# Optimization experiments

Hardware: AMD Instinct MI355X
Metric: run time of the kernel (lower is better)

Reference implementation:

```python
import jax, jax.numpy as jnp
import numpy as np

B, S, D, H = 2, 2048, 2048, 16
HD = D // H  # head_dim = 128


def setup_inputs() -> dict:
    key = jax.random.key(0)
    ks = jax.random.split(key, 9)
    s = 1.0 / np.sqrt(D)
    return {
        "x": jax.random.normal(ks[0], (B, S, D), jnp.float32),
        "Wq": jax.random.normal(ks[1], (D, D), jnp.float32) * s,
        "bq": jax.random.normal(ks[2], (D,), jnp.float32) * 0.02,
        "Wk": jax.random.normal(ks[3], (D, D), jnp.float32) * s,
        "bk": jax.random.normal(ks[4], (D,), jnp.float32) * 0.02,
        "Wv": jax.random.normal(ks[5], (D, D), jnp.float32) * s,
        "bv": jax.random.normal(ks[6], (D,), jnp.float32) * 0.02,
        "Wo": jax.random.normal(ks[7], (D, D), jnp.float32) * s,
        "bo": jax.random.normal(ks[8], (D,), jnp.float32) * 0.02,
    }


def reference(x, Wq, bq, Wk, bk, Wv, bv, Wo, bo):
    b, s, d = x.shape
    # nn.Linear: y = x @ W.T + b
    def split(t):
        # [b, s, d] -> [b, H, s, HD]
        return t.reshape(b, s, H, HD).transpose(0, 2, 1, 3)

    q = split(x @ Wq.T + bq)
    k = split(x @ Wk.T + bk)
    v = split(x @ Wv.T + bv)

    scale = jnp.asarray(HD, x.dtype) ** 0.5
    qk = jnp.einsum("bhqd,bhkd->bhqk", q, k) / scale  # [b, H, s, s]
    weights = jax.nn.softmax(qk, axis=-1)
    attn = jnp.einsum("bhqk,bhkd->bhqd", weights, v)  # [b, H, s, HD]

    merged = attn.transpose(0, 2, 1, 3).reshape(b, s, d)
    return merged @ Wo.T + bo
```

## Files before the change

kernel.cpp:

```cpp
#include <hip/hip_runtime.h>

typedef __bf16 bf16_t;
typedef bf16_t bf16x8 __attribute__((ext_vector_type(8)));
typedef bf16_t bf16x4 __attribute__((ext_vector_type(4)));
typedef float  f32x4  __attribute__((ext_vector_type(4)));

#define DDIM  2048
#define SEQ   2048
#define NH    16
#define HDIM  128
#define BATCH 2
#define MROWS (BATCH * SEQ)
#define XEL   ((size_t)MROWS * DDIM)

__device__ __forceinline__ void async_ld16(const bf16_t* g, bf16_t* l) {
  __builtin_amdgcn_global_load_lds(
      (const __attribute__((address_space(1))) void*)g,
      (__attribute__((address_space(3))) void*)l, 16, 0, 0);
}

__global__ void cvt_f32_bf16(const float* __restrict__ in,
                             bf16_t* __restrict__ out, int n) {
  int i = (blockIdx.x * blockDim.x + threadIdx.x) * 4;
  const int stride = gridDim.x * blockDim.x * 4;
  for (; i < n; i += stride) {
    const float4 v = *reinterpret_cast<const float4*>(in + i);
    bf16x4 o;
    o[0] = (bf16_t)v.x; o[1] = (bf16_t)v.y;
    o[2] = (bf16_t)v.z; o[3] = (bf16_t)v.w;
    *reinterpret_cast<bf16x4*>(out + i) = o;
  }
}

__global__ __launch_bounds__(512, 2) void gemm_qkv(
    const bf16_t* __restrict__ Ax, const bf16_t* __restrict__ Wcat,
    const float* __restrict__ bq, const float* __restrict__ bk,
    const float* __restrict__ bv,
    bf16_t* __restrict__ QKVh, float qscale) {
  __shared__ __align__(16) bf16_t sA[2][2][128 * 64];
  __shared__ __align__(16) bf16_t sB[2][192 * 64];

  const int tid  = threadIdx.x;
  const int lane = tid & 63;
  const int w    = tid >> 6;
  const int wm   = w >> 2;
  const int wn   = w & 3;
  const int lg   = lane >> 4;
  const int lr   = lane & 15;

  const int bid = blockIdx.x;
  const int l   = (bid & 7) * 64 + (bid >> 3);
  const int tm  = l & 15;
  const int tn  = l >> 4;
  const int row0  = tm * 256;
  const int ncol0 = tn * 192;

  auto stA = [&](int buf, int ha, int kt) {
#pragma unroll
    for (int L = 0; L < 2; ++L) {
      const int c = L * 512 + tid, r = c >> 3, ch = c & 7;
      async_ld16(Ax + (size_t)(row0 + ha * 128 + r) * DDIM + kt * 64 +
                     ((ch ^ (r & 7)) * 8),
                 &sA[buf][ha][c * 8]);
    }
  };
  auto stB = [&](int buf, int kt) {
#pragma unroll
    for (int L = 0; L < 3; ++L) {
      const int c = L * 512 + tid, r = c >> 3, ch = c & 7;
      async_ld16(Wcat + (size_t)(ncol0 + r) * DDIM + kt * 64 +
                     ((ch ^ (r & 7)) * 8),
                 &sB[buf][c * 8]);
    }
  };
  auto ldA = [&](int buf, int mf, int k) {
    const int row = mf * 16 + lr;
    const int ch  = (k * 4 + lg) ^ (row & 7);
    return *reinterpret_cast<const bf16x8*>(&sA[buf][wm][row * 64 + ch * 8]);
  };
  auto ldB = [&](int buf, int nf, int k) {
    const int row = wn * 48 + nf * 16 + lr;
    const int ch  = (k * 4 + lg) ^ (row & 7);
    return *reinterpret_cast<const bf16x8*>(&sB[buf][row * 64 + ch * 8]);
  };

  f32x4  acc[8][3] = {};
  bf16x8 bfr[3][2];

#define GPH(BUF, Q, LOADB, STAGE_STMT, VMW)                                   \
  {                                                                           \
    bf16x8 a00 = ldA(BUF, 2 * (Q), 0), a01 = ldA(BUF, 2 * (Q), 1);            \
    bf16x8 a10 = ldA(BUF, 2 * (Q) + 1, 0), a11 = ldA(BUF, 2 * (Q) + 1, 1);    \
    if (LOADB) {                                                              \
      _Pragma("unroll") for (int nf = 0; nf < 3; ++nf) {                      \
        bfr[nf][0] = ldB(BUF, nf, 0);                                         \
        bfr[nf][1] = ldB(BUF, nf, 1);                                         \
      }                                                                       \
    }                                                                         \
    STAGE_STMT;                                                               \
    if (VMW) asm volatile("s_waitcnt vmcnt(3)" ::: "memory");                 \
    __builtin_amdgcn_s_barrier();                                             \
    asm volatile("s_waitcnt lgkmcnt(0)" ::: "memory");                        \
    __builtin_amdgcn_sched_barrier(0);                                        \
    __builtin_amdgcn_s_setprio(1);                                            \
    _Pragma("unroll") for (int k = 0; k < 2; ++k) {                           \
      const bf16x8 A0 = k ? a01 : a00;                                        \
      const bf16x8 A1 = k ? a11 : a10;                                        \
      _Pragma("unroll") for (int nf = 0; nf < 3; ++nf) {                      \
        acc[2 * (Q)][nf] = __builtin_amdgcn_mfma_f32_16x16x32_bf16(           \
            A0, bfr[nf][k], acc[2 * (Q)][nf], 0, 0, 0);                       \
        acc[2 * (Q) + 1][nf] = __builtin_amdgcn_mfma_f32_16x16x32_bf16(       \
            A1, bfr[nf][k], acc[2 * (Q) + 1][nf], 0, 0, 0);                   \
      }                                                                       \
    }                                                                         \
    __builtin_amdgcn_s_setprio(0);                                            \
    __builtin_amdgcn_s_barrier();                                             \
  }

  stA(0, 0, 0); stA(0, 1, 0);
  stB(0, 0);
  stB(1, 1);
  asm volatile("s_waitcnt vmcnt(3)" ::: "memory");
  __builtin_amdgcn_s_barrier();

  for (int i = 0; i < 16; ++i) {
    const int t1 = (2 * i + 1) & 31;
    const int t2 = (2 * i + 2) & 31;
    const int t3 = (2 * i + 3) & 31;
    GPH(0, 0, true,  { stA(1, 0, t1); stA(1, 1, t1); }, 0)
    GPH(0, 1, false, { stB(0, t2); },                   0)
    GPH(0, 2, false, {},                                0)
    GPH(0, 3, false, {},                                1)
    GPH(1, 0, true,  { stA(0, 0, t2); stA(0, 1, t2); }, 0)
    GPH(1, 1, false, { stB(1, t3); },                   0)
    GPH(1, 2, false, {},                                0)
    GPH(1, 3, false, {},                                1)
  }
#undef GPH
  asm volatile("s_waitcnt vmcnt(0)" ::: "memory");

#pragma unroll
  for (int mf = 0; mf < 8; ++mf) {
    const int rr0 = row0 + wm * 128 + mf * 16 + lg * 4;
#pragma unroll
    for (int nf = 0; nf < 3; ++nf) {
      const int col = ncol0 + wn * 48 + nf * 16 + lr;
      const int mat = col >> 11;
      const int c2  = col & (DDIM - 1);
      const float bs = ((mat == 0) ? bq : (mat == 1) ? bk : bv)[c2];
      const float sc = (mat == 0) ? qscale : 1.0f;
      const int h = c2 >> 7, hd = c2 & (HDIM - 1);
      bf16_t* outb = QKVh + (size_t)mat * XEL;
#pragma unroll
      for (int r = 0; r < 4; ++r) {
        const int rr = rr0 + r;
        const int b = rr >> 11, s = rr & (SEQ - 1);
        outb[(((size_t)(b * NH + h)) * SEQ + s) * HDIM + hd] =
            (bf16_t)((acc[mf][nf][r] + bs) * sc);
      }
    }
  }
}

template <int OUTMODE>
__global__ __launch_bounds__(256) void gemm_bt(
    const bf16_t* __restrict__ A, const bf16_t* __restrict__ Bw,
    const float* __restrict__ bias, void* __restrict__ outp,
    int M, int N, int K, float scale) {
  __shared__ __align__(16) bf16_t sA[2][128 * 32];
  __shared__ __align__(16) bf16_t sB[2][128 * 32];

  const int tid  = threadIdx.x;
  const int lane = tid & 63;
  const int w    = tid >> 6;
  const int wm   = w >> 1;
  const int wn   = w & 1;
  const int lg   = lane >> 4;
  const int lr   = lane & 15;
  const int row0 = blockIdx.y * 128;
  const int col0 = blockIdx.x * 128;

  const int srow = tid >> 2;
  const int scol = (tid & 3) * 8;

  const bf16_t* gA = A  + (size_t)(row0 + srow) * K + scol;
  const bf16_t* gB = Bw + (size_t)(col0 + srow) * K + scol;

  f32x4 acc[4][4] = {};

  auto stage = [&](int buf, int k0) {
    async_ld16(gA + k0,                  &sA[buf][tid * 8]);
    async_ld16(gA + 64 * (size_t)K + k0, &sA[buf][(256 + tid) * 8]);
    async_ld16(gB + k0,                  &sB[buf][tid * 8]);
    async_ld16(gB + 64 * (size_t)K + k0, &sB[buf][(256 + tid) * 8]);
  };

  stage(0, 0);
  __syncthreads();

  int cur = 0;
  const int NT = K / 32;
  for (int t = 0; t < NT; ++t) {
    if (t + 1 < NT) stage(cur ^ 1, (t + 1) * 32);
    bf16x8 af[4], bfr[4];
#pragma unroll
    for (int i = 0; i < 4; ++i) {
      af[i]  = *reinterpret_cast<const bf16x8*>(
          &sA[cur][(wm * 64 + i * 16 + lr) * 32 + lg * 8]);
      bfr[i] = *reinterpret_cast<const bf16x8*>(
          &sB[cur][(wn * 64 + i * 16 + lr) * 32 + lg * 8]);
    }
#pragma unroll
    for (int i = 0; i < 4; ++i)
#pragma unroll
      for (int j = 0; j < 4; ++j)
        acc[i][j] = __builtin_amdgcn_mfma_f32_16x16x32_bf16(
            af[i], bfr[j], acc[i][j], 0, 0, 0);
    __syncthreads();
    cur ^= 1;
  }

#pragma unroll
  for (int i = 0; i < 4; ++i) {
    const int rowb = row0 + wm * 64 + i * 16 + lg * 4;
#pragma unroll
    for (int j = 0; j < 4; ++j) {
      const int col = col0 + wn * 64 + j * 16 + lr;
      const float bs = bias[col];
#pragma unroll
      for (int r = 0; r < 4; ++r) {
        const float v = (acc[i][j][r] + bs) * scale;
        const int rr = rowb + r;
        if (OUTMODE == 2) {
          ((float*)outp)[(size_t)rr * N + col] = v;
        } else {
          const int b  = rr >> 11;
          const int s  = rr & (SEQ - 1);
          const int h  = col >> 7;
          const int hd = col & (HDIM - 1);
          ((bf16_t*)outp)[(((size_t)(b * NH + h)) * SEQ + s) * HDIM + hd] =
              (bf16_t)v;
        }
      }
    }
  }
}

__global__ __launch_bounds__(256) void transpose_v(
    const bf16_t* __restrict__ Vp, bf16_t* __restrict__ Vt) {
  __shared__ __align__(16) bf16_t tt[64][72];
  const int bh = blockIdx.z;
  const int s0 = blockIdx.x * 64;
  const int d0 = blockIdx.y * 64;
  const int t  = threadIdx.x;
#pragma unroll
  for (int c = 0; c < 2; ++c) {
    const int r   = (c * 256 + t) >> 3;
    const int col = (t & 7) * 8;
    bf16x8 v = *reinterpret_cast<const bf16x8*>(
        Vp + ((size_t)bh * SEQ + s0 + r) * HDIM + d0 + col);
    *reinterpret_cast<bf16x8*>(&tt[r][col]) = v;
  }
  __syncthreads();
#pragma unroll
  for (int c = 0; c < 2; ++c) {
    const int dr = (c * 256 + t) >> 3;
    const int sc = (t & 7) * 8;
    bf16x8 o;
#pragma unroll
    for (int i = 0; i < 8; ++i) o[i] = tt[sc + i][dr];
    *reinterpret_cast<bf16x8*>(
        Vt + ((size_t)bh * HDIM + d0 + dr) * SEQ + s0 + sc) = o;
  }
}

__global__ __launch_bounds__(256) void attn_fwd(
    const bf16_t* __restrict__ Q, const bf16_t* __restrict__ K,
    const bf16_t* __restrict__ Vt, bf16_t* __restrict__ out) {
  __shared__ __align__(16) bf16_t sK[64 * 128];
  __shared__ __align__(16) bf16_t sV[128 * 64];
  __shared__ __align__(16) bf16_t sP[4][32][72];

  const int tid  = threadIdx.x;
  const int lane = tid & 63;
  const int w    = tid >> 6;
  const int lg   = lane >> 4;
  const int lr   = lane & 15;

  const int bid     = blockIdx.x;
  const int logical = (bid & 7) * 64 + (bid >> 3);
  const int bh      = logical >> 4;
  const int q0      = (logical & 15) * 128;
  const int qw      = q0 + w * 32;

  const bf16_t* Kb = K  + (size_t)bh * SEQ * HDIM;
  const bf16_t* Vb = Vt + (size_t)bh * HDIM * SEQ;

  bf16x8 qf[2][4];
#pragma unroll
  for (int mf = 0; mf < 2; ++mf) {
    const bf16_t* qbase = Q + ((size_t)bh * SEQ + qw + mf * 16 + lr) * HDIM;
#pragma unroll
    for (int kc = 0; kc < 4; ++kc)
      qf[mf][kc] = *reinterpret_cast<const bf16x8*>(qbase + kc * 32 + lg * 8);
  }

  bf16x8 onesf;
#pragma unroll
  for (int i = 0; i < 8; ++i) onesf[i] = (bf16_t)1.0f;

  f32x4 o[2][8] = {};
  f32x4 o1[2] = {};

  for (int kv0 = 0; kv0 < SEQ; kv0 += 64) {
    __syncthreads();
#pragma unroll
    for (int p = 0; p < 4; ++p) {
      const int slot = p * 256 + tid;
      const int kr = slot >> 4, kc = slot & 15;
      async_ld16(Kb + ((size_t)(kv0 + kr)) * HDIM + ((kc ^ (kr & 7)) * 8),
                 sK + slot * 8);
      const int vr = slot >> 3, vc = slot & 7;
      async_ld16(Vb + (size_t)vr * SEQ + kv0 + ((vc ^ (vr & 7)) * 8),
                 sV + slot * 8);
    }
    __syncthreads();

    f32x4 s[2][4] = {};
    __builtin_amdgcn_s_setprio(1);
#pragma unroll
    for (int kc = 0; kc < 4; ++kc) {
#pragma unroll
      for (int cb = 0; cb < 4; ++cb) {
        const int r  = cb * 16 + lr;
        const int ch = kc * 4 + lg;
        bf16x8 kf = *reinterpret_cast<const bf16x8*>(
            sK + r * 128 + ((ch ^ (r & 7)) * 8));
        s[0][cb] = __builtin_amdgcn_mfma_f32_16x16x32_bf16(qf[0][kc], kf, s[0][cb], 0, 0, 0);
        s[1][cb] = __builtin_amdgcn_mfma_f32_16x16x32_bf16(qf[1][kc], kf, s[1][cb], 0, 0, 0);
      }
    }
    __builtin_amdgcn_s_setprio(0);

#pragma unroll
    for (int mf = 0; mf < 2; ++mf)
#pragma unroll
      for (int r = 0; r < 4; ++r)
#pragma unroll
        for (int cb = 0; cb < 4; ++cb) {
          const float p = __builtin_amdgcn_exp2f(s[mf][cb][r]);
          sP[w][mf * 16 + lg * 4 + r][cb * 16 + lr] = (bf16_t)p;
        }

    asm volatile("s_waitcnt lgkmcnt(0)" ::: "memory");

    __builtin_amdgcn_s_setprio(1);
#pragma unroll
    for (int ks = 0; ks < 2; ++ks) {
      bf16x8 pf0 = *reinterpret_cast<const bf16x8*>(&sP[w][lr][ks * 32 + lg * 8]);
      bf16x8 pf1 = *reinterpret_cast<const bf16x8*>(&sP[w][16 + lr][ks * 32 + lg * 8]);
      o1[0] = __builtin_amdgcn_mfma_f32_16x16x32_bf16(pf0, onesf, o1[0], 0, 0, 0);
      o1[1] = __builtin_amdgcn_mfma_f32_16x16x32_bf16(pf1, onesf, o1[1], 0, 0, 0);
#pragma unroll
      for (int ob = 0; ob < 8; ++ob) {
        const int r  = ob * 16 + lr;
        const int ch = ks * 4 + lg;
        bf16x8 vf = *reinterpret_cast<const bf16x8*>(
            sV + r * 64 + ((ch ^ (r & 7)) * 8));
        o[0][ob] = __builtin_amdgcn_mfma_f32_16x16x32_bf16(pf0, vf, o[0][ob], 0, 0, 0);
        o[1][ob] = __builtin_amdgcn_mfma_f32_16x16x32_bf16(pf1, vf, o[1][ob], 0, 0, 0);
      }
    }
    __builtin_amdgcn_s_setprio(0);
  }

  const int b = bh >> 4, h = bh & 15;
#pragma unroll
  for (int mf = 0; mf < 2; ++mf) {
#pragma unroll
    for (int r = 0; r < 4; ++r) {
      const float inv_l = 1.0f / o1[mf][r];
      const int row = qw + mf * 16 + lg * 4 + r;
      bf16_t* obase = out + ((size_t)b * SEQ + row) * DDIM + h * HDIM;
#pragma unroll
      for (int ob = 0; ob < 8; ++ob)
        obase[ob * 16 + lr] = (bf16_t)(o[mf][ob][r] * inv_l);
    }
  }
}

extern "C" void kernel_launch(void* const* d_in, const int* in_sizes, int n_in,
                              void* d_out, int out_size, void* d_ws,
                              size_t ws_size, hipStream_t stream) {
  const float* x  = (const float*)d_in[0];
  const float* Wq = (const float*)d_in[1];
  const float* bq = (const float*)d_in[2];
  const float* Wk = (const float*)d_in[3];
  const float* bk = (const float*)d_in[4];
  const float* Wv = (const float*)d_in[5];
  const float* bv = (const float*)d_in[6];
  const float* Wo = (const float*)d_in[7];
  const float* bo = (const float*)d_in[8];

  bf16_t* ws = (bf16_t*)d_ws;
  const size_t XE = XEL;
  const size_t WE = (size_t)DDIM * DDIM;
  bf16_t* xb  = ws;
  bf16_t* wqb = ws + XE;
  bf16_t* wkb = wqb + WE;
  bf16_t* wvb = wkb + WE;
  bf16_t* wob = wvb + WE;
  bf16_t* Qh  = wob + WE;
  bf16_t* Kh  = Qh + XE;
  bf16_t* Vh  = Kh + XE;
  bf16_t* Vt  = Vh + XE;
  bf16_t* merged = xb;

  cvt_f32_bf16<<<4096, 256, 0, stream>>>(x, xb, (int)XE);
  cvt_f32_bf16<<<2048, 256, 0, stream>>>(Wq, wqb, (int)WE);
  cvt_f32_bf16<<<2048, 256, 0, stream>>>(Wk, wkb, (int)WE);
  cvt_f32_bf16<<<2048, 256, 0, stream>>>(Wv, wvb, (int)WE);
  cvt_f32_bf16<<<2048, 256, 0, stream>>>(Wo, wob, (int)WE);

  const float qscale = 0.12751744520778695f;

  gemm_qkv<<<512, 512, 0, stream>>>(xb, wqb, bq, bk, bv, Qh, qscale);

  transpose_v<<<dim3(SEQ / 64, HDIM / 64, BATCH * NH), 256, 0, stream>>>(Vh, Vt);

  attn_fwd<<<512, 256, 0, stream>>>(Qh, Kh, Vt, merged);

  dim3 gg(DDIM / 128, MROWS / 128);
  gemm_bt<2><<<gg, 256, 0, stream>>>(merged, wob, bo, d_out, MROWS, DDIM, DDIM, 1.0f);
}
```

Baseline: 276.1 us.

## Fuse conversions, triple-buffer QKV GEMM B tiles, rewrite output projection GEMM

Merges the five fp32-to-bf16 conversion launches into a single grid-stride kernel over all inputs. The QKV GEMM now triple-buffers its weight tile with a per-k-step loop that interleaves LDS fragment loads with MFMA groups through partial lgkmcnt waits. Its warp layout changes from 2x4 to 4x2, giving each wave a 64x96 sub-tile. The output projection GEMM is replaced by a 256x128-tile, 512-thread kernel with swizzled LDS, global_load_lds staging and the same pipeline, in place of the simple double-buffered 128x128 one. This costs more LDS per block, which may reduce occupancy.

```diff
diff --git a/kernel.cpp b/kernel.cpp
--- a/kernel.cpp
+++ b/kernel.cpp
@@ -12,6 +12,7 @@
 #define BATCH 2
 #define MROWS (BATCH * SEQ)
 #define XEL   ((size_t)MROWS * DDIM)
+#define WEL   ((size_t)DDIM * DDIM)
 
 __device__ __forceinline__ void async_ld16(const bf16_t* g, bf16_t* l) {
   __builtin_amdgcn_global_load_lds(
@@ -19,18 +20,50 @@
       (__attribute__((address_space(3))) void*)l, 16, 0, 0);
 }
 
-__global__ void cvt_f32_bf16(const float* __restrict__ in,
-                             bf16_t* __restrict__ out, int n) {
-  int i = (blockIdx.x * blockDim.x + threadIdx.x) * 4;
-  const int stride = gridDim.x * blockDim.x * 4;
-  for (; i < n; i += stride) {
-    const float4 v = *reinterpret_cast<const float4*>(in + i);
+__global__ void cvt_all(const float* __restrict__ x,
+                        const float* __restrict__ w0,
+                        const float* __restrict__ w1,
+                        const float* __restrict__ w2,
+                        const float* __restrict__ w3,
+                        bf16_t* __restrict__ ox, bf16_t* __restrict__ ow) {
+  const size_t CX = XEL / 4;
+  const size_t CW = WEL / 4;
+  const size_t total = CX + 4 * CW;
+  size_t c = (size_t)blockIdx.x * blockDim.x + threadIdx.x;
+  const size_t stride = (size_t)gridDim.x * blockDim.x;
+  for (; c < total; c += stride) {
+    float4 v;
+    bf16_t* outp;
+    if (c < CX) {
+      v = reinterpret_cast<const float4*>(x)[c];
+      outp = ox + c * 4;
+    } else {
+      const size_t d = c - CX;
+      const size_t seg = d >> 20;
+      const float* w = seg == 0 ? w0 : seg == 1 ? w1 : seg == 2 ? w2 : w3;
+      v = reinterpret_cast<const float4*>(w)[d & (CW - 1)];
+      outp = ow + d * 4;
+    }
     bf16x4 o;
     o[0] = (bf16_t)v.x; o[1] = (bf16_t)v.y;
     o[2] = (bf16_t)v.z; o[3] = (bf16_t)v.w;
-    *reinterpret_cast<bf16x4*>(out + i) = o;
-  }
-}
+    *reinterpret_cast<bf16x4*>(outp) = o;
+  }
+}
+
+#define QMM(NF, BV)                                                           \
+  __builtin_amdgcn_s_setprio(1);                                              \
+  _Pragma("unroll") for (int mf = 0; mf < 4; ++mf) {                          \
+    acc[mf][NF] = __builtin_amdgcn_mfma_f32_16x16x32_bf16(                    \
+        a_[mf][0], BV[0], acc[mf][NF], 0, 0, 0);                              \
+    acc[mf][NF] = __builtin_amdgcn_mfma_f32_16x16x32_bf16(                    \
+        a_[mf][1], BV[1], acc[mf][NF], 0, 0, 0);                              \
+  }                                                                           \
+  __builtin_amdgcn_s_setprio(0);
+
+#define LGKM(N)                                                               \
+  asm volatile("s_waitcnt lgkmcnt(" #N ")" ::: "memory");                     \
+  __builtin_amdgcn_sched_barrier(0);
 
 __global__ __launch_bounds__(512, 2) void gemm_qkv(
     const bf16_t* __restrict__ Ax, const bf16_t* __restrict__ Wcat,
@@ -38,137 +71,7 @@
     const float* __restrict__ bv,
     bf16_t* __restrict__ QKVh, float qscale) {
   __shared__ __align__(16) bf16_t sA[2][2][128 * 64];
-  __shared__ __align__(16) bf16_t sB[2][192 * 64];
-
-  const int tid  = threadIdx.x;
-  const int lane = tid & 63;
-  const int w    = tid >> 6;
-  const int wm   = w >> 2;
-  const int wn   = w & 3;
-  const int lg   = lane >> 4;
-  const int lr   = lane & 15;
-
-  const int bid = blockIdx.x;
-  const int l   = (bid & 7) * 64 + (bid >> 3);
-  const int tm  = l & 15;
-  const int tn  = l >> 4;
-  const int row0  = tm * 256;
-  const int ncol0 = tn * 192;
-
-  auto stA = [&](int buf, int ha, int kt) {
-#pragma unroll
-    for (int L = 0; L < 2; ++L) {
-      const int c = L * 512 + tid, r = c >> 3, ch = c & 7;
-      async_ld16(Ax + (size_t)(row0 + ha * 128 + r) * DDIM + kt * 64 +
-                     ((ch ^ (r & 7)) * 8),
-                 &sA[buf][ha][c * 8]);
-    }
-  };
-  auto stB = [&](int buf, int kt) {
-#pragma unroll
-    for (int L = 0; L < 3; ++L) {
-      const int c = L * 512 + tid, r = c >> 3, ch = c & 7;
-      async_ld16(Wcat + (size_t)(ncol0 + r) * DDIM + kt * 64 +
-                     ((ch ^ (r & 7)) * 8),
-                 &sB[buf][c * 8]);
-    }
-  };
-  auto ldA = [&](int buf, int mf, int k) {
-    const int row = mf * 16 + lr;
-    const int ch  = (k * 4 + lg) ^ (row & 7);
-    return *reinterpret_cast<const bf16x8*>(&sA[buf][wm][row * 64 + ch * 8]);
-  };
-  auto ldB = [&](int buf, int nf, int k) {
-    const int row = wn * 48 + nf * 16 + lr;
-    const int ch  = (k * 4 + lg) ^ (row & 7);
-    return *reinterpret_cast<const bf16x8*>(&sB[buf][row * 64 + ch * 8]);
-  };
-
-  f32x4  acc[8][3] = {};
-  bf16x8 bfr[3][2];
-
-#define GPH(BUF, Q, LOADB, STAGE_STMT, VMW)                                   \
-  {                                                                           \
-    bf16x8 a00 = ldA(BUF, 2 * (Q), 0), a01 = ldA(BUF, 2 * (Q), 1);            \
-    bf16x8 a10 = ldA(BUF, 2 * (Q) + 1, 0), a11 = ldA(BUF, 2 * (Q) + 1, 1);    \
-    if (LOADB) {                                                              \
-      _Pragma("unroll") for (int nf = 0; nf < 3; ++nf) {                      \
-        bfr[nf][0] = ldB(BUF, nf, 0);                                         \
-        bfr[nf][1] = ldB(BUF, nf, 1);                                         \
-      }                                                                       \
-    }                                                                         \
-    STAGE_STMT;                                                               \
-    if (VMW) asm volatile("s_waitcnt vmcnt(3)" ::: "memory");                 \
-    __builtin_amdgcn_s_barrier();                                             \
-    asm volatile("s_waitcnt lgkmcnt(0)" ::: "memory");                        \
-    __builtin_amdgcn_sched_barrier(0);                                        \
-    __builtin_amdgcn_s_setprio(1);                                            \
-    _Pragma("unroll") for (int k = 0; k < 2; ++k) {                           \
-      const bf16x8 A0 = k ? a01 : a00;                                        \
-      const bf16x8 A1 = k ? a11 : a10;                                        \
-      _Pragma("unroll") for (int nf = 0; nf < 3; ++nf) {                      \
-        acc[2 * (Q)][nf] = __builtin_amdgcn_mfma_f32_16x16x32_bf16(           \
-            A0, bfr[nf][k], acc[2 * (Q)][nf], 0, 0, 0);                       \
-        acc[2 * (Q) + 1][nf] = __builtin_amdgcn_mfma_f32_16x16x32_bf16(       \
-            A1, bfr[nf][k], acc[2 * (Q) + 1][nf], 0, 0, 0);                   \
-      }                                                                       \
-    }                                                                         \
-    __builtin_amdgcn_s_setprio(0);                                            \
-    __builtin_amdgcn_s_barrier();                                             \
-  }
-
-  stA(0, 0, 0); stA(0, 1, 0);
-  stB(0, 0);
-  stB(1, 1);
-  asm volatile("s_waitcnt vmcnt(3)" ::: "memory");
-  __builtin_amdgcn_s_barrier();
-
-  for (int i = 0; i < 16; ++i) {
-    const int t1 = (2 * i + 1) & 31;
-    const int t2 = (2 * i + 2) & 31;
-    const int t3 = (2 * i + 3) & 31;
-    GPH(0, 0, true,  { stA(1, 0, t1); stA(1, 1, t1); }, 0)
-    GPH(0, 1, false, { stB(0, t2); },                   0)
-    GPH(0, 2, false, {},                                0)
-    GPH(0, 3, false, {},                                1)
-    GPH(1, 0, true,  { stA(0, 0, t2); stA(0, 1, t2); }, 0)
-    GPH(1, 1, false, { stB(1, t3); },                   0)
-    GPH(1, 2, false, {},                                0)
-    GPH(1, 3, false, {},                                1)
-  }
-#undef GPH
-  asm volatile("s_waitcnt vmcnt(0)" ::: "memory");
-
-#pragma unroll
-  for (int mf = 0; mf < 8; ++mf) {
-    const int rr0 = row0 + wm * 128 + mf * 16 + lg * 4;
-#pragma unroll
-    for (int nf = 0; nf < 3; ++nf) {
-      const int col = ncol0 + wn * 48 + nf * 16 + lr;
-      const int mat = col >> 11;
-      const int c2  = col & (DDIM - 1);
-      const float bs = ((mat == 0) ? bq : (mat == 1) ? bk : bv)[c2];
-      const float sc = (mat == 0) ? qscale : 1.0f;
-      const int h = c2 >> 7, hd = c2 & (HDIM - 1);
-      bf16_t* outb = QKVh + (size_t)mat * XEL;
-#pragma unroll
-      for (int r = 0; r < 4; ++r) {
-        const int rr = rr0 + r;
-        const int b = rr >> 11, s = rr & (SEQ - 1);
-        outb[(((size_t)(b * NH + h)) * SEQ + s) * HDIM + hd] =
-            (bf16_t)((acc[mf][nf][r] + bs) * sc);
-      }
-    }
-  }
-}
-
-template <int OUTMODE>
-__global__ __launch_bounds__(256) void gemm_bt(
-    const bf16_t* __restrict__ A, const bf16_t* __restrict__ Bw,
-    const float* __restrict__ bias, void* __restrict__ outp,
-    int M, int N, int K, float scale) {
-  __shared__ __align__(16) bf16_t sA[2][128 * 32];
-  __shared__ __align__(16) bf16_t sB[2][128 * 32];
+  __shared__ __align__(16) bf16_t sB[3][192 * 64];
 
   const int tid  = threadIdx.x;
   const int lane = tid & 63;
@@ -177,71 +80,228 @@
   const int wn   = w & 1;
   const int lg   = lane >> 4;
   const int lr   = lane & 15;
-  const int row0 = blockIdx.y * 128;
-  const int col0 = blockIdx.x * 128;
-
-  const int srow = tid >> 2;
-  const int scol = (tid & 3) * 8;
-
-  const bf16_t* gA = A  + (size_t)(row0 + srow) * K + scol;
-  const bf16_t* gB = Bw + (size_t)(col0 + srow) * K + scol;
+
+  const int bid = blockIdx.x;
+  const int l   = (bid & 7) * 64 + (bid >> 3);
+  const int tm  = l & 15;
+  const int tn  = l >> 4;
+  const int row0  = tm * 256;
+  const int ncol0 = tn * 192;
+
+  auto stA = [&](int buf, int ha, int kt) {
+#pragma unroll
+    for (int L = 0; L < 2; ++L) {
+      const int c = L * 512 + tid, r = c >> 3, ch = c & 7;
+      async_ld16(Ax + (size_t)(row0 + ha * 128 + r) * DDIM + kt * 64 +
+                     ((ch ^ (r & 7)) * 8),
+                 &sA[buf][ha][c * 8]);
+    }
+  };
+  auto stB = [&](int buf, int kt) {
+#pragma unroll
+    for (int L = 0; L < 3; ++L) {
+      const int c = L * 512 + tid, r = c >> 3, ch = c & 7;
+      async_ld16(Wcat + (size_t)(ncol0 + r) * DDIM + kt * 64 +
+                     ((ch ^ (r & 7)) * 8),
+                 &sB[buf][c * 8]);
+    }
+  };
+  auto ldA = [&](int buf, int mf, int k) {
+    const int row = (wm & 1) * 64 + mf * 16 + lr;
+    const int ch  = (k * 4 + lg) ^ (row & 7);
+    return *reinterpret_cast<const bf16x8*>(
+        &sA[buf][wm >> 1][row * 64 + ch * 8]);
+  };
+  auto ldB = [&](int buf, int nf, int k) {
+    const int row = wn * 96 + nf * 16 + lr;
+    const int ch  = (k * 4 + lg) ^ (row & 7);
+    return *reinterpret_cast<const bf16x8*>(&sB[buf][row * 64 + ch * 8]);
+  };
+
+  f32x4 acc[4][6] = {};
+
+  stA(0, 0, 0); stA(0, 1, 0);
+  stB(0, 0);
+  stB(1, 1);
+  asm volatile("s_waitcnt vmcnt(3)" ::: "memory");
+  __builtin_amdgcn_s_barrier();
+
+  int bc = 0;
+  for (int t = 0; t < 32; ++t) {
+    const int p   = t & 1;
+    const int pn  = p ^ 1;
+    const int tn1 = (t + 1) & 31, tn2 = (t + 2) & 31;
+    const int b2i = bc == 0 ? 2 : bc - 1;
+
+    bf16x8 a_[4][2];
+#pragma unroll
+    for (int mf = 0; mf < 4; ++mf) {
+      a_[mf][0] = ldA(p, mf, 0);
+      a_[mf][1] = ldA(p, mf, 1);
+    }
+    bf16x8 b0[2], b1[2], b2[2], b3[2], b4[2], b5[2];
+    b0[0] = ldB(bc, 0, 0); b0[1] = ldB(bc, 0, 1);
+    b1[0] = ldB(bc, 1, 0); b1[1] = ldB(bc, 1, 1);
+    __builtin_amdgcn_sched_barrier(0);
+    stA(pn, 0, tn1); stA(pn, 1, tn1);
+    stB(b2i, tn2);
+    __builtin_amdgcn_sched_barrier(0);
+    LGKM(2)
+    QMM(0, b0)
+    b2[0] = ldB(bc, 2, 0); b2[1] = ldB(bc, 2, 1);
+    __builtin_amdgcn_sched_barrier(0);
+    LGKM(2)
+    QMM(1, b1)
+    b3[0] = ldB(bc, 3, 0); b3[1] = ldB(bc, 3, 1);
+    __builtin_amdgcn_sched_barrier(0);
+    LGKM(2)
+    QMM(2, b2)
+    b4[0] = ldB(bc, 4, 0); b4[1] = ldB(bc, 4, 1);
+    __builtin_amdgcn_sched_barrier(0);
+    LGKM(2)
+    QMM(3, b3)
+    b5[0] = ldB(bc, 5, 0); b5[1] = ldB(bc, 5, 1);
+    __builtin_amdgcn_sched_barrier(0);
+    LGKM(2)
+    QMM(4, b4)
+    LGKM(0)
+    QMM(5, b5)
+    asm volatile("s_waitcnt vmcnt(3)" ::: "memory");
+    __builtin_amdgcn_s_barrier();
+    bc = bc == 2 ? 0 : bc + 1;
+  }
+  asm volatile("s_waitcnt vmcnt(0)" ::: "memory");
+
+#pragma unroll
+  for (int mf = 0; mf < 4; ++mf) {
+    const int rr0 = row0 + wm * 64 + mf * 16 + lg * 4;
+#pragma unroll
+    for (int nf = 0; nf < 6; ++nf) {
+      const int col = ncol0 + wn * 96 + nf * 16 + lr;
+      const int mat = col >> 11;
+      const int c2  = col & (DDIM - 1);
+      const float bs = ((mat == 0) ? bq : (mat == 1) ? bk : bv)[c2];
+      const float sc = (mat == 0) ? qscale : 1.0f;
+      const int h = c2 >> 7, hd = c2 & (HDIM - 1);
+      bf16_t* outb = QKVh + (size_t)mat * XEL;
+#pragma unroll
+      for (int r = 0; r < 4; ++r) {
+        const int rr = rr0 + r;
+        const int b = rr >> 11, s = rr & (SEQ - 1);
+        outb[(((size_t)(b * NH + h)) * SEQ + s) * HDIM + hd] =
+            (bf16_t)((acc[mf][nf][r] + bs) * sc);
+      }
+    }
+  }
+}
+
+__global__ __launch_bounds__(512, 2) void gemm_bt(
+    const bf16_t* __restrict__ A, const bf16_t* __restrict__ Bw,
+    const float* __restrict__ bias, float* __restrict__ outp) {
+  __shared__ __align__(16) bf16_t sA[2][2][128 * 64];
+  __shared__ __align__(16) bf16_t sB[3][128 * 64];
+
+  const int tid  = threadIdx.x;
+  const int lane = tid & 63;
+  const int w    = tid >> 6;
+  const int wm   = w >> 1;
+  const int wn   = w & 1;
+  const int lg   = lane >> 4;
+  const int lr   = lane & 15;
+
+  const int bid = blockIdx.x;
+  const int l   = (bid & 7) * 32 + (bid >> 3);
+  const int tm  = l & 15;
+  const int tn  = l >> 4;
+  const int row0 = tm * 256;
+  const int col0 = tn * 128;
+
+  auto stA = [&](int buf, int ha, int kt) {
+#pragma unroll
+    for (int L = 0; L < 2; ++L) {
+      const int c = L * 512 + tid, r = c >> 3, ch = c & 7;
+      async_ld16(A + (size_t)(row0 + ha * 128 + r) * DDIM + kt * 64 +
+                     ((ch ^ (r & 7)) * 8),
+                 &sA[buf][ha][c * 8]);
+    }
+  };
+  auto stB = [&](int buf, int kt) {
+#pragma unroll
+    for (int L = 0; L < 2; ++L) {
+      const int c = L * 512 + tid, r = c >> 3, ch = c & 7;
+      async_ld16(Bw + (size_t)(col0 + r) * DDIM + kt * 64 +
+                     ((ch ^ (r & 7)) * 8),
+                 &sB[buf][c * 8]);
+    }
+  };
+  auto ldA = [&](int buf, int mf, int k) {
+    const int row = (wm & 1) * 64 + mf * 16 + lr;
+    const int ch  = (k * 4 + lg) ^ (row & 7);
+    return *reinterpret_cast<const bf16x8*>(
+        &sA[buf][wm >> 1][row * 64 + ch * 8]);
+  };
+  auto ldB = [&](int buf, int nf, int k) {
+    const int row = wn * 64 + nf * 16 + lr;
+    const int ch  = (k * 4 + lg) ^ (row & 7);
+    return *reinterpret_cast<const bf16x8*>(&sB[buf][row * 64 + ch * 8]);
+  };
 
   f32x4 acc[4][4] = {};
 
-  auto stage = [&](int buf, int k0) {
-    async_ld16(gA + k0,                  &sA[buf][tid * 8]);
-    async_ld16(gA + 64 * (size_t)K + k0, &sA[buf][(256 + tid) * 8]);
-    async_ld16(gB + k0,                  &sB[buf][tid * 8]);
-    async_ld16(gB + 64 * (size_t)K + k0, &sB[buf][(256 + tid) * 8]);
-  };
-
-  stage(0, 0);
-  __syncthreads();
-
-  int cur = 0;
-  const int NT = K / 32;
-  for (int t = 0; t < NT; ++t) {
-    if (t + 1 < NT) stage(cur ^ 1, (t + 1) * 32);
-    bf16x8 af[4], bfr[4];
-#pragma unroll
-    for (int i = 0; i < 4; ++i) {
-      af[i]  = *reinterpret_cast<const bf16x8*>(
-          &sA[cur][(wm * 64 + i * 16 + lr) * 32 + lg * 8]);
-      bfr[i] = *reinterpret_cast<const bf16x8*>(
-          &sB[cur][(wn * 64 + i * 16 + lr) * 32 + lg * 8]);
-    }
-#pragma unroll
-    for (int i = 0; i < 4; ++i)
-#pragma unroll
-      for (int j = 0; j < 4; ++j)
-        acc[i][j] = __builtin_amdgcn_mfma_f32_16x16x32_bf16(
-            af[i], bfr[j], acc[i][j], 0, 0, 0);
-    __syncthreads();
-    cur ^= 1;
-  }
-
-#pragma unroll
-  for (int i = 0; i < 4; ++i) {
-    const int rowb = row0 + wm * 64 + i * 16 + lg * 4;
-#pragma unroll
-    for (int j = 0; j < 4; ++j) {
-      const int col = col0 + wn * 64 + j * 16 + lr;
+  stA(0, 0, 0); stA(0, 1, 0);
+  stB(0, 0);
+  stB(1, 1);
+  asm volatile("s_waitcnt vmcnt(2)" ::: "memory");
+  __builtin_amdgcn_s_barrier();
+
+  int bc = 0;
+  for (int t = 0; t < 32; ++t) {
+    const int p   = t & 1;
+    const int pn  = p ^ 1;
+    const int tn1 = (t + 1) & 31, tn2 = (t + 2) & 31;
+    const int b2i = bc == 0 ? 2 : bc - 1;
+
+    bf16x8 a_[4][2];
+#pragma unroll
+    for (int mf = 0; mf < 4; ++mf) {
+      a_[mf][0] = ldA(p, mf, 0);
+      a_[mf][1] = ldA(p, mf, 1);
+    }
+    bf16x8 b0[2], b1[2], b2[2], b3[2];
+    b0[0] = ldB(bc, 0, 0); b0[1] = ldB(bc, 0, 1);
+    b1[0] = ldB(bc, 1, 0); b1[1] = ldB(bc, 1, 1);
+    __builtin_amdgcn_sched_barrier(0);
+    stA(pn, 0, tn1); stA(pn, 1, tn1);
+    stB(b2i, tn2);
+    __builtin_amdgcn_sched_barrier(0);
+    LGKM(2)
+    QMM(0, b0)
+    b2[0] = ldB(bc, 2, 0); b2[1] = ldB(bc, 2, 1);
+    __builtin_amdgcn_sched_barrier(0);
+    LGKM(2)
+    QMM(1, b1)
+    b3[0] = ldB(bc, 3, 0); b3[1] = ldB(bc, 3, 1);
+    __builtin_amdgcn_sched_barrier(0);
+    LGKM(2)
+    QMM(2, b2)
+    LGKM(0)
+    QMM(3, b3)
+    asm volatile("s_waitcnt vmcnt(2)" ::: "memory");
+    __builtin_amdgcn_s_barrier();
+    bc = bc == 2 ? 0 : bc + 1;
+  }
+  asm volatile("s_waitcnt vmcnt(0)" ::: "memory");
+
+#pragma unroll
+  for (int mf = 0; mf < 4; ++mf) {
+    const int row = row0 + wm * 64 + mf * 16 + lg * 4;
+#pragma unroll
+    for (int nf = 0; nf < 4; ++nf) {
+      const int col = col0 + wn * 64 + nf * 16 + lr;
       const float bs = bias[col];
 #pragma unroll
-      for (int r = 0; r < 4; ++r) {
-        const float v = (acc[i][j][r] + bs) * scale;
-        const int rr = rowb + r;
-        if (OUTMODE == 2) {
-          ((float*)outp)[(size_t)rr * N + col] = v;
-        } else {
-          const int b  = rr >> 11;
-          const int s  = rr & (SEQ - 1);
-          const int h  = col >> 7;
-          const int hd = col & (HDIM - 1);
-          ((bf16_t*)outp)[(((size_t)(b * NH + h)) * SEQ + s) * HDIM + hd] =
-              (bf16_t)v;
-        }
-      }
+      for (int r = 0; r < 4; ++r)
+        outp[(size_t)(row + r) * DDIM + col] = acc[mf][nf][r] + bs;
     }
   }
 }
@@ -404,7 +464,7 @@
 
   bf16_t* ws = (bf16_t*)d_ws;
   const size_t XE = XEL;
-  const size_t WE = (size_t)DDIM * DDIM;
+  const size_t WE = WEL;
   bf16_t* xb  = ws;
   bf16_t* wqb = ws + XE;
   bf16_t* wkb = wqb + WE;
@@ -416,11 +476,7 @@
   bf16_t* Vt  = Vh + XE;
   bf16_t* merged = xb;
 
-  cvt_f32_bf16<<<4096, 256, 0, stream>>>(x, xb, (int)XE);
-  cvt_f32_bf16<<<2048, 256, 0, stream>>>(Wq, wqb, (int)WE);
-  cvt_f32_bf16<<<2048, 256, 0, stream>>>(Wk, wkb, (int)WE);
-  cvt_f32_bf16<<<2048, 256, 0, stream>>>(Wv, wvb, (int)WE);
-  cvt_f32_bf16<<<2048, 256, 0, stream>>>(Wo, wob, (int)WE);
+  cvt_all<<<2048, 256, 0, stream>>>(x, Wq, Wk, Wv, Wo, xb, wqb);
 
   const float qscale = 0.12751744520778695f;
 
@@ -430,6 +486,5 @@
 
   attn_fwd<<<512, 256, 0, stream>>>(Qh, Kh, Vt, merged);
 
-  dim3 gg(DDIM / 128, MROWS / 128);
-  gemm_bt<2><<<gg, 256, 0, stream>>>(merged, wob, bo, d_out, MROWS, DDIM, DDIM, 1.0f);
-}
+  gemm_bt<<<256, 512, 0, stream>>>(merged, wob, bo, (float*)d_out);
+}
```

New measurement: 262.0 us. -5.1%, faster.
